# Kernel tuning notes

Hardware: AMD Instinct MI355X
Metric: run time of the kernel (lower is better)

The kernel has to match this reference:

```python
import jax, jax.numpy as jnp
import numpy as np

NUM_Q = 124      # num_of_questions (2*124 == 248 hardcoded in the module)
MAX_STEP = 512   # max_step
B = 2048         # number of students


def setup_inputs() -> dict:
    key = jax.random.key(0)
    k1, k2, k3, k4 = jax.random.split(key, 4)
    # predictions in (0,1) as expected by BCE
    pred = jax.random.uniform(k1, (B, MAX_STEP, NUM_Q), jnp.float32, 0.01, 0.99)
    # per-student valid sequence length; remaining steps are zero padding
    lengths = jax.random.randint(k2, (B,), MAX_STEP // 4, MAX_STEP)
    q = jax.random.randint(k3, (B, MAX_STEP), 0, NUM_Q)        # question id per step
    c = jax.random.randint(k4, (B, MAX_STEP), 0, 2)            # 1 = correct, 0 = incorrect
    col = q + (1 - c) * NUM_Q                                   # correct -> first half, incorrect -> second half
    step_mask = (jnp.arange(MAX_STEP)[None, :] < lengths[:, None]).astype(jnp.float32)
    batch = jax.nn.one_hot(col, 2 * NUM_Q, dtype=jnp.float32) * step_mask[..., None]
    return {"pred": pred, "batch": batch}


def reference(pred, batch):
    Q = NUM_Q
    T = MAX_STEP
    b = (batch >= 1).astype(pred.dtype)                 # torch.where(batch>=1, 1., 0.)
    delta = b[..., :Q] + b[..., Q:2 * Q]                # [B, T, Q] one-hot of answered question
    # diag(pred[:T-1] @ delta[1:].T) per student == rowwise dot product
    p = jnp.einsum('btq,btq->bt', pred[:, :T - 1], delta[:, 1:])  # [B, T-1]
    # ((correct - incorrect).sum(1) + 1) // 2  -> 1 if correct, 0 if incorrect/padding
    a = jnp.floor(((b[..., :Q] - b[..., Q:2 * Q]).sum(-1) + 1.0) / 2.0)[:, 1:]  # [B, T-1]
    # dynamic truncation: keep prefix up to last index with p > 0 (full length if none)
    idx = jnp.arange(T - 1)
    last = jnp.max(jnp.where(p > 0, idx, -1), axis=1)   # [B]
    L = jnp.where(last >= 0, last + 1, T - 1)           # [B] effective length
    mask = idx[None, :] < L[:, None]                    # [B, T-1]
    maskf = mask.astype(pred.dtype)
    # BCE with torch-style log clamping at -100; masked positions use dummy 0.5
    p_safe = jnp.where(mask, p, 0.5)
    lp = jnp.maximum(jnp.log(p_safe), -100.0)
    l1p = jnp.maximum(jnp.log(1.0 - p_safe), -100.0)
    bce = -(a * lp + (1.0 - a) * l1p)
    # loss = sum over students of mean BCE over that student's truncated length
    loss = jnp.sum(jnp.sum(bce * maskf, axis=1) / L.astype(pred.dtype))
    # original concatenates ragged p/a; we return fixed-shape masked versions
    return loss, p * maskf, a * maskf
```

## Files before the change

### kernel.cpp

```cpp
#include <hip/hip_runtime.h>

#define NUM_Q    124
#define TWO_Q    248
#define MAX_STEP 512
#define TM1      511
#define V4_PER_ROW 62

__global__ __launch_bounds__(256) void scan_kernel(
    const float4* __restrict__ batch4, int* __restrict__ cols, unsigned n4)
{
    unsigned stride = gridDim.x * 256u;
    for (unsigned i = blockIdx.x * 256u + threadIdx.x; i < n4; i += stride) {
        float4 v = batch4[i];
        if (v.x >= 1.f || v.y >= 1.f || v.z >= 1.f || v.w >= 1.f) {
            unsigned row  = i / V4_PER_ROW;
            unsigned base = (i - row * V4_PER_ROW) * 4u;
            int col = (v.x >= 1.f) ? (int)base
                    : (v.y >= 1.f) ? (int)base + 1
                    : (v.z >= 1.f) ? (int)base + 2
                    : (int)base + 3;
            cols[row] = col;
        }
    }
}

__global__ __launch_bounds__(256) void loss_kernel(
    const float* __restrict__ pred, const int* __restrict__ cols,
    float* __restrict__ out, int B)
{
    int b   = blockIdx.x;
    int tid = threadIdx.x;
    const int*   crow = cols + (size_t)b * MAX_STEP;
    const float* prow = pred + (size_t)b * MAX_STEP * NUM_Q;

    int t0 = tid, t1 = tid + 256;
    float p0 = 0.f, p1 = 0.f, a0 = 0.f, a1 = 0.f;
    int local_last = -1;

    {
        int col = crow[t0 + 1];
        if (col >= 0) {
            int q = (col < NUM_Q) ? col : (col - NUM_Q);
            a0 = (col < NUM_Q) ? 1.f : 0.f;
            p0 = prow[(size_t)t0 * NUM_Q + q];
            if (p0 > 0.f) local_last = t0;
        }
    }
    if (t1 < TM1) {
        int col = crow[t1 + 1];
        if (col >= 0) {
            int q = (col < NUM_Q) ? col : (col - NUM_Q);
            a1 = (col < NUM_Q) ? 1.f : 0.f;
            p1 = prow[(size_t)t1 * NUM_Q + q];
            if (p1 > 0.f) local_last = t1;
        }
    }

    __shared__ int   s_last[4];
    __shared__ float s_sum[4];
    #pragma unroll
    for (int off = 32; off > 0; off >>= 1) {
        int o = __shfl_down(local_last, off, 64);
        local_last = (o > local_last) ? o : local_last;
    }
    int wid = tid >> 6;
    if ((tid & 63) == 0) s_last[wid] = local_last;
    __syncthreads();
    int last = max(max(s_last[0], s_last[1]), max(s_last[2], s_last[3]));
    int L = (last >= 0) ? (last + 1) : TM1;

    float* out_p = out + 1 + (size_t)b * TM1;
    float* out_a = out + 1 + (size_t)B * TM1 + (size_t)b * TM1;

    float sum = 0.f;
    {
        bool m = (t0 < L);
        out_p[t0] = m ? p0 : 0.f;
        out_a[t0] = m ? a0 : 0.f;
        if (m) {
            float lp  = fmaxf(logf(p0),       -100.f);
            float l1p = fmaxf(logf(1.f - p0), -100.f);
            sum += -(a0 * lp + (1.f - a0) * l1p);
        }
    }
    if (t1 < TM1) {
        bool m = (t1 < L);
        out_p[t1] = m ? p1 : 0.f;
        out_a[t1] = m ? a1 : 0.f;
        if (m) {
            float lp  = fmaxf(logf(p1),       -100.f);
            float l1p = fmaxf(logf(1.f - p1), -100.f);
            sum += -(a1 * lp + (1.f - a1) * l1p);
        }
    }

    #pragma unroll
    for (int off = 32; off > 0; off >>= 1)
        sum += __shfl_down(sum, off, 64);
    if ((tid & 63) == 0) s_sum[wid] = sum;
    __syncthreads();
    if (tid == 0) {
        float tot = s_sum[0] + s_sum[1] + s_sum[2] + s_sum[3];
        atomicAdd(out, tot / (float)L);
    }
}

extern "C" void kernel_launch(void* const* d_in, const int* in_sizes, int n_in,
                              void* d_out, int out_size, void* d_ws, size_t ws_size,
                              hipStream_t stream)
{
    const float* pred  = (const float*)d_in[0];
    const float* batch = (const float*)d_in[1];
    float* out = (float*)d_out;
    int*   cols = (int*)d_ws;

    int B = in_sizes[0] / (MAX_STEP * NUM_Q);
    int nrows = B * MAX_STEP;
    unsigned n4 = (unsigned)nrows * V4_PER_ROW;

    hipMemsetAsync(cols, 0xFF, (size_t)nrows * sizeof(int), stream);
    hipMemsetAsync(d_out, 0, sizeof(float), stream);

    scan_kernel<<<4096, 256, 0, stream>>>((const float4*)batch, cols, n4);

    loss_kernel<<<B, 256, 0, stream>>>(pred, cols, out, B);
}
```

Baseline: 1.514 ms.

## Fuse batch scan into loss kernel using shared-memory column buffer

Merges the one-hot scan kernel and the loss kernel into one per-student kernel. Each block scans its own student's batch rows, stores the column index per step in shared memory, then does the gather and BCE reduction. This removes the workspace memset, the global cols write/read and one kernel launch. In exchange, each wave loops serially over 128 rows with only 62 of 64 lanes active, which may reduce memory-level parallelism compared with the grid-stride scan.

```diff
diff --git a/kernel.cpp b/kernel.cpp
--- a/kernel.cpp
+++ b/kernel.cpp
@@ -6,39 +6,48 @@
 #define TM1      511
 #define V4_PER_ROW 62
 
-__global__ __launch_bounds__(256) void scan_kernel(
-    const float4* __restrict__ batch4, int* __restrict__ cols, unsigned n4)
+__global__ __launch_bounds__(256) void fused_loss_kernel(
+    const float* __restrict__ pred, const float* __restrict__ batch,
+    float* __restrict__ out, int B)
 {
-    unsigned stride = gridDim.x * 256u;
-    for (unsigned i = blockIdx.x * 256u + threadIdx.x; i < n4; i += stride) {
-        float4 v = batch4[i];
-        if (v.x >= 1.f || v.y >= 1.f || v.z >= 1.f || v.w >= 1.f) {
-            unsigned row  = i / V4_PER_ROW;
-            unsigned base = (i - row * V4_PER_ROW) * 4u;
-            int col = (v.x >= 1.f) ? (int)base
-                    : (v.y >= 1.f) ? (int)base + 1
-                    : (v.z >= 1.f) ? (int)base + 2
-                    : (int)base + 3;
-            cols[row] = col;
+    __shared__ int   scols[MAX_STEP];
+    __shared__ int   s_last[4];
+    __shared__ float s_sum[4];
+
+    int b    = blockIdx.x;
+    int tid  = threadIdx.x;
+    int wid  = tid >> 6;
+    int lane = tid & 63;
+
+    scols[tid]       = -1;
+    scols[tid + 256] = -1;
+    __syncthreads();
+
+    const float4* brow4 = (const float4*)(batch + (size_t)b * MAX_STEP * TWO_Q);
+    if (lane < V4_PER_ROW) {
+        int base = lane * 4;
+        #pragma unroll 4
+        for (int i = 0; i < 128; ++i) {
+            int t = wid * 128 + i;
+            float4 v = brow4[(size_t)t * V4_PER_ROW + lane];
+            if (v.x >= 1.f || v.y >= 1.f || v.z >= 1.f || v.w >= 1.f) {
+                int col = (v.x >= 1.f) ? base
+                        : (v.y >= 1.f) ? base + 1
+                        : (v.z >= 1.f) ? base + 2
+                        : base + 3;
+                scols[t] = col;
+            }
         }
     }
-}
+    __syncthreads();
 
-__global__ __launch_bounds__(256) void loss_kernel(
-    const float* __restrict__ pred, const int* __restrict__ cols,
-    float* __restrict__ out, int B)
-{
-    int b   = blockIdx.x;
-    int tid = threadIdx.x;
-    const int*   crow = cols + (size_t)b * MAX_STEP;
     const float* prow = pred + (size_t)b * MAX_STEP * NUM_Q;
-
     int t0 = tid, t1 = tid + 256;
     float p0 = 0.f, p1 = 0.f, a0 = 0.f, a1 = 0.f;
     int local_last = -1;
 
     {
-        int col = crow[t0 + 1];
+        int col = scols[t0 + 1];
         if (col >= 0) {
             int q = (col < NUM_Q) ? col : (col - NUM_Q);
             a0 = (col < NUM_Q) ? 1.f : 0.f;
@@ -47,7 +56,7 @@
         }
     }
     if (t1 < TM1) {
-        int col = crow[t1 + 1];
+        int col = scols[t1 + 1];
         if (col >= 0) {
             int q = (col < NUM_Q) ? col : (col - NUM_Q);
             a1 = (col < NUM_Q) ? 1.f : 0.f;
@@ -56,15 +65,12 @@
         }
     }
 
-    __shared__ int   s_last[4];
-    __shared__ float s_sum[4];
     #pragma unroll
     for (int off = 32; off > 0; off >>= 1) {
         int o = __shfl_down(local_last, off, 64);
         local_last = (o > local_last) ? o : local_last;
     }
-    int wid = tid >> 6;
-    if ((tid & 63) == 0) s_last[wid] = local_last;
+    if (lane == 0) s_last[wid] = local_last;
     __syncthreads();
     int last = max(max(s_last[0], s_last[1]), max(s_last[2], s_last[3]));
     int L = (last >= 0) ? (last + 1) : TM1;
@@ -97,7 +103,7 @@
     #pragma unroll
     for (int off = 32; off > 0; off >>= 1)
         sum += __shfl_down(sum, off, 64);
-    if ((tid & 63) == 0) s_sum[wid] = sum;
+    if (lane == 0) s_sum[wid] = sum;
     __syncthreads();
     if (tid == 0) {
         float tot = s_sum[0] + s_sum[1] + s_sum[2] + s_sum[3];
@@ -112,16 +118,10 @@
     const float* pred  = (const float*)d_in[0];
     const float* batch = (const float*)d_in[1];
     float* out = (float*)d_out;
-    int*   cols = (int*)d_ws;
 
     int B = in_sizes[0] / (MAX_STEP * NUM_Q);
-    int nrows = B * MAX_STEP;
-    unsigned n4 = (unsigned)nrows * V4_PER_ROW;
 
-    hipMemsetAsync(cols, 0xFF, (size_t)nrows * sizeof(int), stream);
     hipMemsetAsync(d_out, 0, sizeof(float), stream);
 
-    scan_kernel<<<4096, 256, 0, stream>>>((const float4*)batch, cols, n4);
-
-    loss_kernel<<<B, 256, 0, stream>>>(pred, cols, out, B);
+    fused_loss_kernel<<<B, 256, 0, stream>>>(pred, batch, out, B);
 }
```

New measurement: 1.498 ms. No clear change (-1.1%).
